# Optimization experiments

Hardware: AMD Instinct MI355X
Metric: run time of the kernel (lower is better)

The kernel has to match this reference:

```python
import jax, jax.numpy as jnp
import numpy as np

B, S, H, NH = 4, 2048, 512, 8
HD = H // NH  # head dim = 64


def setup_inputs() -> dict:
    key = jax.random.key(0)
    ks = jax.random.split(key, 12)
    f = lambda k, sh: jax.random.normal(k, sh, dtype=jnp.float32)
    w = lambda k: f(k, (H, H)) * 0.02  # Linear weight (out, in), torch-style
    return {
        "q": f(ks[0], (B, S, H)),
        "k": f(ks[1], (B, S, H)),
        "v": f(ks[2], (B, S, H)),
        "mask": jax.random.randint(ks[3], (B, S, S), 0, 2, dtype=jnp.int32),
        "Wq": w(ks[4]), "bq": jnp.zeros((H,), jnp.float32),
        "Wk": w(ks[5]), "bk": jnp.zeros((H,), jnp.float32),
        "Wv": w(ks[6]), "bv": jnp.zeros((H,), jnp.float32),
        "Wo": w(ks[7]), "bo": jnp.zeros((H,), jnp.float32),
    }


def reference(q, k, v, mask, Wq, bq, Wk, bk, Wv, bv, Wo, bo):
    b, s, h = q.shape
    scale = jnp.asarray(np.sqrt(HD), q.dtype)
    # QKV projections (torch Linear: x @ W.T + b), split into heads: b n s h
    def heads(x, W, bias):
        y = x @ W.T + bias
        return y.reshape(b, s, NH, HD).transpose(0, 2, 1, 3)
    Q = heads(q, Wq, bq)
    K = heads(k, Wk, bk)
    V = heads(v, Wv, bv)
    scores = jnp.einsum('bnsh,bnth->bnst', Q, K) / scale
    scores = jnp.where(mask[:, None, :, :] == 0, jnp.asarray(-1e9, scores.dtype), scores)
    attn = jax.nn.softmax(scores, axis=-1)
    # dropout is identity in eval mode
    out = jnp.einsum('bnst,bnth->bnsh', attn, V)
    out = out.transpose(0, 2, 1, 3).reshape(b, s, h)
    return out @ Wo.T + bo
```

## Files before the change

kernel.cpp:

```cpp
#include <hip/hip_runtime.h>
#include <cstdint>


typedef __bf16 bf16x8 __attribute__((ext_vector_type(8)));
typedef float  f32x4  __attribute__((ext_vector_type(4)));
typedef float  f32x16 __attribute__((ext_vector_type(16)));
typedef unsigned int uint32x2 __attribute__((ext_vector_type(2)));

#define MFMA16(a, b, c) __builtin_amdgcn_mfma_f32_16x16x32_bf16(a, b, c, 0, 0, 0)
#define MFMA32(a, b, c) __builtin_amdgcn_mfma_f32_32x32x16_bf16(a, b, c, 0, 0, 0)

__device__ __forceinline__ ushort f2bf(float f) {
  union { float f; uint32_t u; } v; v.f = f;
  return (ushort)((v.u + 0x8000u) >> 16);
}
__device__ __forceinline__ uint packbf(float a, float b) {
  union { float f; uint32_t u; } x, y; x.f = a; y.f = b;
#if __has_builtin(__builtin_amdgcn_perm)
  return __builtin_amdgcn_perm(y.u + 0x8000u, x.u + 0x8000u, 0x07060302u);
#else
  return ((x.u + 0x8000u) >> 16) | ((y.u + 0x8000u) & 0xffff0000u);
#endif
}
__device__ __forceinline__ uint cvtpk(float a, float b) {
  uint r;
  asm("v_cvt_pk_bf16_f32 %0, %1, %2" : "=v"(r) : "v"(a), "v"(b));
  return r;
}
__device__ __forceinline__ float exp2r(float x) {
#if __has_builtin(__builtin_amdgcn_exp2f)
  return __builtin_amdgcn_exp2f(x);
#else
  return exp2f(x);
#endif
}

typedef const __attribute__((address_space(1))) unsigned int* gas_u32;
typedef __attribute__((address_space(3))) unsigned int* las_u32;
__device__ __forceinline__ void gll16(const void* g, void* l) {
  __builtin_amdgcn_global_load_lds((gas_u32)g, (las_u32)l, 16, 0, 0);
}

__global__ __launch_bounds__(256) void cvt_w(
    const float* __restrict__ w0, const float* __restrict__ w1,
    const float* __restrict__ w2, const float* __restrict__ w3,
    ushort* __restrict__ dst) {
  const float* src = (blockIdx.y == 0) ? w0 : (blockIdx.y == 1) ? w1
                   : (blockIdx.y == 2) ? w2 : w3;
  ushort* d = dst + (size_t)blockIdx.y * 262144;
  int i = blockIdx.x * 256 + threadIdx.x;
  for (int j = i; j < 65536; j += 16384) {
    float4 v = ((const float4*)src)[j];
    uint2 o = { packbf(v.x, v.y), packbf(v.z, v.w) };
    ((uint2*)d)[j] = o;
  }
}

__global__ __launch_bounds__(256) void mask_bits_kernel(
    const int* __restrict__ mask, unsigned long long* __restrict__ MB) {
  const int lane = threadIdx.x & 63;
  const int wv = (int)((blockIdx.x * 256 + threadIdx.x) >> 6);
  const size_t base = (size_t)wv * 64;
  for (int j = 0; j < 64; j += 4) {
    int v0 = mask[(base + j + 0) * 64 + lane];
    int v1 = mask[(base + j + 1) * 64 + lane];
    int v2 = mask[(base + j + 2) * 64 + lane];
    int v3 = mask[(base + j + 3) * 64 + lane];
    unsigned long long b0 = __ballot(v0 != 0), b1 = __ballot(v1 != 0);
    unsigned long long b2 = __ballot(v2 != 0), b3 = __ballot(v3 != 0);
    if (lane == 0) {
      MB[base + j] = b0; MB[base + j + 1] = b1;
      MB[base + j + 2] = b2; MB[base + j + 3] = b3;
    }
  }
}

__global__ __launch_bounds__(256, 3) void qkv_gemm(
    const float* __restrict__ q, const float* __restrict__ k,
    const float* __restrict__ v, const ushort* __restrict__ Wb,
    const float* __restrict__ bq, const float* __restrict__ bk,
    const float* __restrict__ bv, ushort* __restrict__ Qh,
    ushort* __restrict__ Kh, ushort* __restrict__ Vt) {
  __shared__ ushort SH[128 * 136];
  __shared__ ushort Ws[128 * 64];
  float* Asf = (float*)SH;
  const int z = blockIdx.z;
  const float* X = (z == 0) ? q : (z == 1) ? k : v;
  const ushort* W = Wb + (size_t)z * 262144;
  const float* bias = (z == 0) ? bq : (z == 1) ? bk : bv;
  const float scale = (z == 0) ? 0.18033688011112042f : 1.0f;
  ushort* Y = (z == 0) ? Qh : (z == 1) ? Kh : Vt;

  const int tid = threadIdx.x, wv = tid >> 6, l = tid & 63;
  const int quad = l >> 4, ln = l & 15;
  const int m0 = blockIdx.x * 128, n0 = blockIdx.y * 128;
  const int wm = (wv & 1) * 64, wn = (wv >> 1) * 64;
  const int srA = l >> 4, sA = l & 15, cA = sA >> 1, hA = sA & 1;
  const int srW = l >> 3, scW = l & 7;
  f32x4 acc[4][4] = {};

  for (int kk = 0; kk < 512; kk += 64) {
#pragma unroll
    for (int i = 0; i < 8; ++i) {
      int rowa = wv * 32 + i * 4 + srA;
      gll16(X + (size_t)(m0 + rowa) * 512 + kk + ((cA ^ (rowa & 7)) * 8 + hA * 4),
            Asf + (wv * 32 + i * 4) * 64);
    }
#pragma unroll
    for (int i = 0; i < 4; ++i) {
      int roww = wv * 32 + i * 8 + srW;
      gll16(W + (size_t)(n0 + roww) * 512 + kk + ((scW ^ (roww & 7)) * 8),
            Ws + (wv * 32 + i * 8) * 64);
    }
    __syncthreads();
#pragma unroll
    for (int ks = 0; ks < 2; ++ks) {
      bf16x8 a[4], bw[4];
#pragma unroll
      for (int mt = 0; mt < 4; ++mt) {
        int row = wm + mt * 16 + ln;
        int p = (ks * 4 + quad) ^ (row & 7);
        const float* ap = &Asf[row * 64 + p * 8];
        f32x4 x0 = *(const f32x4*)ap;
        f32x4 x1 = *(const f32x4*)(ap + 4);
        union { uint u[4]; bf16x8 v; } t;
        t.u[0] = cvtpk(x0[0], x0[1]);
        t.u[1] = cvtpk(x0[2], x0[3]);
        t.u[2] = cvtpk(x1[0], x1[1]);
        t.u[3] = cvtpk(x1[2], x1[3]);
        a[mt] = t.v;
      }
#pragma unroll
      for (int nt = 0; nt < 4; ++nt) {
        int row = wn + nt * 16 + ln;
        bw[nt] = *(const bf16x8*)&Ws[row * 64 + (((ks * 4 + quad) ^ (row & 7)) * 8)];
      }
#pragma unroll
      for (int mt = 0; mt < 4; ++mt)
#pragma unroll
        for (int nt = 0; nt < 4; ++nt)
          acc[mt][nt] = MFMA16(a[mt], bw[nt], acc[mt][nt]);
    }
    __syncthreads();
  }
  float bval[4];
#pragma unroll
  for (int nt = 0; nt < 4; ++nt) bval[nt] = bias[n0 + wn + nt * 16 + ln];

  if (z == 2) {
    ushort* uT = SH;
#pragma unroll
    for (int nt = 0; nt < 4; ++nt) {
      int row = wn + nt * 16 + ln;
#pragma unroll
      for (int mt = 0; mt < 4; ++mt) {
        int mbase = wm + mt * 16 + quad * 4;
        uint2 pk = { cvtpk(acc[mt][nt][0] + bval[nt], acc[mt][nt][1] + bval[nt]),
                     cvtpk(acc[mt][nt][2] + bval[nt], acc[mt][nt][3] + bval[nt]) };
        int c = (mbase >> 3) ^ (row & 7);
        *(uint2*)&uT[row * 128 + c * 8 + (quad & 1) * 4] = pk;
      }
    }
    __syncthreads();
#pragma unroll
    for (int j = 0; j < 8; ++j) {
      int i = tid + j * 256;
      int row = i >> 4, cs = i & 15;
      int g = cs ^ (row & 7);
      uint4 d = *(const uint4*)&uT[row * 128 + cs * 8];
      int n = n0 + row, m = m0 + g * 8;
      int bb = m >> 11, s = m & 2047, h = n >> 6, hd = n & 63;
      *(uint4*)(Y + ((size_t)((bb * 8 + h) * 64 + hd)) * 2048 + s) = d;
    }
  } else {
    ushort* uM = SH;
#pragma unroll
    for (int mt = 0; mt < 4; ++mt)
#pragma unroll
      for (int nt = 0; nt < 4; ++nt) {
        int n = wn + nt * 16 + ln;
#pragma unroll
        for (int r = 0; r < 4; ++r) {
          int m = wm + mt * 16 + quad * 4 + r;
          uM[m * 136 + n] = f2bf((acc[mt][nt][r] + bval[nt]) * scale);
        }
      }
    __syncthreads();
#pragma unroll
    for (int j = 0; j < 8; ++j) {
      int i = tid + j * 256;
      int row = i >> 4, cs = i & 15;
      uint4 d = *(const uint4*)&uM[row * 136 + cs * 8];
      int m = m0 + row, n = n0 + cs * 8;
      int bb = m >> 11, s = m & 2047, h = n >> 6, hd = n & 63;
      *(uint4*)(Y + (((size_t)(bb * 8 + h) * 2048) + s) * 64 + hd) = d;
    }
  }
}

__global__ __launch_bounds__(256, 4) void attn(
    const ushort* __restrict__ Qh, const ushort* __restrict__ Kh,
    const ushort* __restrict__ Vt, const unsigned long long* __restrict__ MB,
    ushort* __restrict__ O) {
  __shared__ ushort SMEM[16384];
  ushort* Ks = SMEM;
  ushort* Vs = SMEM + 8192;
  const int tid = threadIdx.x, wv = tid >> 6, lane = tid & 63;
  const int hs = lane >> 5, lq = lane & 31;
  const int qh = wv >> 1, kvh = wv & 1;
  const int bh = blockIdx.x, qb = blockIdx.y;
  const size_t hoff = (size_t)bh * 2048 * 64;
  const int q0 = qb * 64;
  const int qg = q0 + qh * 32 + lq;
  const int srK = lane >> 3, scK = lane & 7;
  const int srV = lane >> 4, scV = lane & 15;

  bf16x8 qf[4];
#pragma unroll
  for (int ki = 0; ki < 4; ++ki)
    qf[ki] = *(const bf16x8*)(Qh + hoff + (size_t)qg * 64 + ki * 16 + hs * 8);

  bf16x8 ones;
#pragma unroll
  for (int j = 0; j < 8; ++j) ones[j] = (__bf16)1.0f;

  f32x16 po0 = {}, po1 = {};
  f32x16 lacc = {};
  const unsigned long long* mrow = MB + ((size_t)(bh >> 3) * 2048 + qg) * 32;

  for (int it = 0; it < 16; ++it) {
    const int kv0 = it * 128;
#pragma unroll
    for (int i = 0; i < 4; ++i) {
      int row = wv * 32 + i * 8 + srK;
      gll16(Kh + hoff + (size_t)(kv0 + row) * 64 + ((scK ^ (row & 7)) * 8),
            Ks + (wv * 32 + i * 8) * 64);
      int rv = wv * 16 + i * 4 + srV;
      gll16(Vt + hoff + (size_t)rv * 2048 + kv0 + ((scV ^ (rv & 7)) * 8),
            Vs + (wv * 16 + i * 4) * 128);
    }
    unsigned long long mbw = mrow[it * 2 + kvh];
    __syncthreads();

#pragma unroll
    for (int ch = 0; ch < 2; ++ch) {
      const int kvb = kvh * 64 + ch * 32;
      f32x16 sc_ = {};
#pragma unroll
      for (int ki = 0; ki < 4; ++ki) {
        int row = kvb + lq;
        bf16x8 ak = *(const bf16x8*)&Ks[row * 64 + (((2 * ki + hs) ^ (row & 7)) * 8)];
        sc_ = MFMA32(ak, qf[ki], sc_);
      }
      uint pk[8];
#pragma unroll
      for (int c = 0; c < 4; ++c) {
        unsigned nib = (unsigned)(mbw >> (ch * 32 + c * 8 + hs * 4)) & 0xFu;
        float p0 = (nib & 1u) ? exp2r(sc_[4 * c + 0]) : 0.f;
        float p1 = (nib & 2u) ? exp2r(sc_[4 * c + 1]) : 0.f;
        float p2 = (nib & 4u) ? exp2r(sc_[4 * c + 2]) : 0.f;
        float p3 = (nib & 8u) ? exp2r(sc_[4 * c + 3]) : 0.f;
        pk[2 * c + 0] = cvtpk(p0, p1);
        pk[2 * c + 1] = cvtpk(p2, p3);
      }
#pragma unroll
      for (int t2 = 0; t2 < 2; ++t2) {
        union { uint u[4]; bf16x8 v; } bp;
#if __has_builtin(__builtin_amdgcn_permlane32_swap)
        uint32x2 r02 = __builtin_amdgcn_permlane32_swap(pk[4 * t2 + 0], pk[4 * t2 + 2], false, false);
        uint32x2 r13 = __builtin_amdgcn_permlane32_swap(pk[4 * t2 + 1], pk[4 * t2 + 3], false, false);
        bp.u[0] = r02[0];
        bp.u[1] = r13[0];
        bp.u[2] = r02[1];
        bp.u[3] = r13[1];
#else
        uint bx0 = (uint)__shfl_xor((int)(hs ? pk[4 * t2 + 0] : pk[4 * t2 + 2]), 32);
        uint bx1 = (uint)__shfl_xor((int)(hs ? pk[4 * t2 + 1] : pk[4 * t2 + 3]), 32);
        bp.u[0] = hs ? bx0 : pk[4 * t2 + 0];
        bp.u[1] = hs ? bx1 : pk[4 * t2 + 1];
        bp.u[2] = hs ? pk[4 * t2 + 2] : bx0;
        bp.u[3] = hs ? pk[4 * t2 + 3] : bx1;
#endif
        lacc = MFMA32(ones, bp.v, lacc);
#pragma unroll
        for (int m2 = 0; m2 < 2; ++m2) {
          int hd = m2 * 32 + lq;
          int gch = (kvb >> 3) + 2 * t2 + hs;
          bf16x8 av = *(const bf16x8*)&Vs[hd * 128 + ((gch ^ (hd & 7)) * 8)];
          if (m2 == 0) po0 = MFMA32(av, bp.v, po0);
          else         po1 = MFMA32(av, bp.v, po1);
        }
      }
    }
    __syncthreads();
  }

  float l_own = lacc[0];
  float* psh = (float*)Ks;
  float* lsh = (float*)Vs;
  ushort* Osh = Vs + 256;
  if (kvh == 1) {
#pragma unroll
    for (int i = 0; i < 16; ++i) psh[(qh * 32 + i) * 64 + lane] = po0[i];
#pragma unroll
    for (int i = 0; i < 16; ++i) psh[(qh * 32 + 16 + i) * 64 + lane] = po1[i];
    lsh[qh * 64 + lane] = l_own;
  }
  __syncthreads();
  if (kvh == 0) {
    float linv = 1.0f / (l_own + lsh[qh * 64 + lane]);
    int row = qh * 32 + lq;
#pragma unroll
    for (int m2 = 0; m2 < 2; ++m2) {
#pragma unroll
      for (int c = 0; c < 4; ++c)
#pragma unroll
        for (int b2 = 0; b2 < 2; ++b2) {
          int r = 4 * c + 2 * b2;
          float v0, v1;
          if (m2 == 0) {
            v0 = (po0[r] + psh[(qh * 32 + r) * 64 + lane]) * linv;
            v1 = (po0[r + 1] + psh[(qh * 32 + r + 1) * 64 + lane]) * linv;
          } else {
            v0 = (po1[r] + psh[(qh * 32 + 16 + r) * 64 + lane]) * linv;
            v1 = (po1[r + 1] + psh[(qh * 32 + 16 + r + 1) * 64 + lane]) * linv;
          }
          int hd = m2 * 32 + 8 * c + 4 * hs + 2 * b2;
          *(uint*)&Osh[row * 72 + hd] = cvtpk(v0, v1);
        }
    }
  }
  __syncthreads();
  for (int i = tid; i < 512; i += 256) {
    int row = i >> 3, cc = i & 7;
    uint4 d = *(const uint4*)&Osh[row * 72 + cc * 8];
    *(uint4*)(O + ((size_t)((bh >> 3) * 2048 + q0 + row)) * 512 +
              (bh & 7) * 64 + cc * 8) = d;
  }
}

__global__ __launch_bounds__(256) void out_gemm(
    const ushort* __restrict__ X, const ushort* __restrict__ W,
    const float* __restrict__ bias, float* __restrict__ Y) {
  __shared__ ushort As[64 * 64];
  __shared__ ushort Ws[128 * 64];
  const int tid = threadIdx.x, wv = tid >> 6, l = tid & 63;
  const int quad = l >> 4, ln = l & 15;
  const int m0 = blockIdx.x * 64, n0 = blockIdx.y * 128;
  const int wm = (wv & 1) * 32, wn = (wv >> 1) * 64;
  const int sr = l >> 3, sc = l & 7;
  f32x4 acc[2][4] = {};
  for (int kk = 0; kk < 512; kk += 64) {
#pragma unroll
    for (int i = 0; i < 2; ++i) {
      int row = wv * 16 + i * 8 + sr;
      gll16(X + (size_t)(m0 + row) * 512 + kk + ((sc ^ (row & 7)) * 8),
            As + (wv * 16 + i * 8) * 64);
    }
#pragma unroll
    for (int i = 0; i < 4; ++i) {
      int row = wv * 32 + i * 8 + sr;
      gll16(W + (size_t)(n0 + row) * 512 + kk + ((sc ^ (row & 7)) * 8),
            Ws + (wv * 32 + i * 8) * 64);
    }
    __syncthreads();
#pragma unroll
    for (int ks = 0; ks < 2; ++ks) {
      bf16x8 a[2], bw[4];
#pragma unroll
      for (int mt = 0; mt < 2; ++mt) {
        int row = wm + mt * 16 + ln;
        a[mt] = *(const bf16x8*)&As[row * 64 + (((ks * 4 + quad) ^ (row & 7)) * 8)];
      }
#pragma unroll
      for (int nt = 0; nt < 4; ++nt) {
        int row = wn + nt * 16 + ln;
        bw[nt] = *(const bf16x8*)&Ws[row * 64 + (((ks * 4 + quad) ^ (row & 7)) * 8)];
      }
#pragma unroll
      for (int mt = 0; mt < 2; ++mt)
#pragma unroll
        for (int nt = 0; nt < 4; ++nt)
          acc[mt][nt] = MFMA16(a[mt], bw[nt], acc[mt][nt]);
    }
    __syncthreads();
  }
#pragma unroll
  for (int mt = 0; mt < 2; ++mt)
#pragma unroll
    for (int nt = 0; nt < 4; ++nt) {
      int n = n0 + wn + nt * 16 + ln;
      float bval = bias[n];
#pragma unroll
      for (int r = 0; r < 4; ++r) {
        int m = m0 + wm + mt * 16 + quad * 4 + r;
        Y[(size_t)m * 512 + n] = acc[mt][nt][r] + bval;
      }
    }
}

extern "C" void kernel_launch(void* const* d_in, const int* in_sizes, int n_in,
                              void* d_out, int out_size, void* d_ws, size_t ws_size,
                              hipStream_t stream) {
  const float* q    = (const float*)d_in[0];
  const float* k    = (const float*)d_in[1];
  const float* v    = (const float*)d_in[2];
  const int*   mask = (const int*)d_in[3];
  const float* Wq   = (const float*)d_in[4];
  const float* bq   = (const float*)d_in[5];
  const float* Wk   = (const float*)d_in[6];
  const float* bk   = (const float*)d_in[7];
  const float* Wv   = (const float*)d_in[8];
  const float* bv   = (const float*)d_in[9];
  const float* Wo   = (const float*)d_in[10];
  const float* bo   = (const float*)d_in[11];
  float* out = (float*)d_out;

  uint8_t* ws = (uint8_t*)d_ws;
  const size_t MiB = 1u << 20;
  ushort* Oh = (ushort*)(ws + 0 * MiB);
  ushort* Qh = (ushort*)(ws + 8 * MiB);
  ushort* Kh = (ushort*)(ws + 16 * MiB);
  ushort* Vt = (ushort*)(ws + 24 * MiB);
  unsigned long long* MB = (unsigned long long*)(ws + 32 * MiB);
  ushort* Wb = (ushort*)(ws + 34 * MiB);

  cvt_w<<<dim3(64, 4), 256, 0, stream>>>(Wq, Wk, Wv, Wo, Wb);
  mask_bits_kernel<<<1024, 256, 0, stream>>>(mask, MB);
  qkv_gemm<<<dim3(64, 4, 3), 256, 0, stream>>>(q, k, v, Wb, bq, bk, bv, Qh, Kh, Vt);
  attn<<<dim3(32, 32), 256, 0, stream>>>(Qh, Kh, Vt, MB, Oh);
  out_gemm<<<dim3(128, 4), 256, 0, stream>>>(Oh, Wb + 3 * 262144, bo, out);
}
```

Before: 251.3 us.

## Pre-convert q/k/v activations to bf16 before the QKV GEMM

Adds a separate pass that converts the fp32 q, k and v inputs to bf16 in workspace, so the QKV GEMM loads bf16 tiles straight into LDS instead of converting fp32 tiles per block. This halves the LDS footprint of the A tile. Launch bounds rise to 4 blocks per CU, and the Q/K epilogue is split into two 64-column halves that fit the smaller shared buffer. The cost is an extra kernel that reads 48 MB of fp32 and writes 24 MB of bf16, which removes the fp32 re-reads each GEMM block did across the four N tiles.

Result: slower. 261.5 us (+4.0%).

```diff
diff --git a/kernel.cpp b/kernel.cpp
--- a/kernel.cpp
+++ b/kernel.cpp
@@ -52,6 +52,19 @@
   for (int j = i; j < 65536; j += 16384) {
     float4 v = ((const float4*)src)[j];
     uint2 o = { packbf(v.x, v.y), packbf(v.z, v.w) };
+    ((uint2*)d)[j] = o;
+  }
+}
+
+__global__ __launch_bounds__(256) void cvt_x(
+    const float* __restrict__ q, const float* __restrict__ k,
+    const float* __restrict__ v, ushort* __restrict__ dst) {
+  const float* src = (blockIdx.y == 0) ? q : (blockIdx.y == 1) ? k : v;
+  ushort* d = dst + (size_t)blockIdx.y * 4194304;
+  int i = blockIdx.x * 256 + threadIdx.x;
+  for (int j = i; j < 1048576; j += 65536) {
+    float4 vv = ((const float4*)src)[j];
+    uint2 o = { cvtpk(vv.x, vv.y), cvtpk(vv.z, vv.w) };
     ((uint2*)d)[j] = o;
   }
 }
@@ -75,17 +88,16 @@
   }
 }
 
-__global__ __launch_bounds__(256, 3) void qkv_gemm(
-    const float* __restrict__ q, const float* __restrict__ k,
-    const float* __restrict__ v, const ushort* __restrict__ Wb,
+__global__ __launch_bounds__(256, 4) void qkv_gemm(
+    const ushort* __restrict__ Xb, const ushort* __restrict__ Wb,
     const float* __restrict__ bq, const float* __restrict__ bk,
     const float* __restrict__ bv, ushort* __restrict__ Qh,
     ushort* __restrict__ Kh, ushort* __restrict__ Vt) {
-  __shared__ ushort SH[128 * 136];
-  __shared__ ushort Ws[128 * 64];
-  float* Asf = (float*)SH;
+  __shared__ ushort SM[16384];
+  ushort* As = SM;
+  ushort* Wt = SM + 8192;
   const int z = blockIdx.z;
-  const float* X = (z == 0) ? q : (z == 1) ? k : v;
+  const ushort* X = Xb + (size_t)z * 4194304;
   const ushort* W = Wb + (size_t)z * 262144;
   const float* bias = (z == 0) ? bq : (z == 1) ? bk : bv;
   const float scale = (z == 0) ? 0.18033688011112042f : 1.0f;
@@ -95,22 +107,17 @@
   const int quad = l >> 4, ln = l & 15;
   const int m0 = blockIdx.x * 128, n0 = blockIdx.y * 128;
   const int wm = (wv & 1) * 64, wn = (wv >> 1) * 64;
-  const int srA = l >> 4, sA = l & 15, cA = sA >> 1, hA = sA & 1;
-  const int srW = l >> 3, scW = l & 7;
+  const int sr = l >> 3, sc = l & 7;
   f32x4 acc[4][4] = {};
 
   for (int kk = 0; kk < 512; kk += 64) {
 #pragma unroll
-    for (int i = 0; i < 8; ++i) {
-      int rowa = wv * 32 + i * 4 + srA;
-      gll16(X + (size_t)(m0 + rowa) * 512 + kk + ((cA ^ (rowa & 7)) * 8 + hA * 4),
-            Asf + (wv * 32 + i * 4) * 64);
-    }
-#pragma unroll
     for (int i = 0; i < 4; ++i) {
-      int roww = wv * 32 + i * 8 + srW;
-      gll16(W + (size_t)(n0 + roww) * 512 + kk + ((scW ^ (roww & 7)) * 8),
-            Ws + (wv * 32 + i * 8) * 64);
+      int row = wv * 32 + i * 8 + sr;
+      gll16(X + (size_t)(m0 + row) * 512 + kk + ((sc ^ (row & 7)) * 8),
+            As + (wv * 32 + i * 8) * 64);
+      gll16(W + (size_t)(n0 + row) * 512 + kk + ((sc ^ (row & 7)) * 8),
+            Wt + (wv * 32 + i * 8) * 64);
     }
     __syncthreads();
 #pragma unroll
@@ -119,21 +126,12 @@
 #pragma unroll
       for (int mt = 0; mt < 4; ++mt) {
         int row = wm + mt * 16 + ln;
-        int p = (ks * 4 + quad) ^ (row & 7);
-        const float* ap = &Asf[row * 64 + p * 8];
-        f32x4 x0 = *(const f32x4*)ap;
-        f32x4 x1 = *(const f32x4*)(ap + 4);
-        union { uint u[4]; bf16x8 v; } t;
-        t.u[0] = cvtpk(x0[0], x0[1]);
-        t.u[1] = cvtpk(x0[2], x0[3]);
-        t.u[2] = cvtpk(x1[0], x1[1]);
-        t.u[3] = cvtpk(x1[2], x1[3]);
-        a[mt] = t.v;
+        a[mt] = *(const bf16x8*)&As[row * 64 + (((ks * 4 + quad) ^ (row & 7)) * 8)];
       }
 #pragma unroll
       for (int nt = 0; nt < 4; ++nt) {
         int row = wn + nt * 16 + ln;
-        bw[nt] = *(const bf16x8*)&Ws[row * 64 + (((ks * 4 + quad) ^ (row & 7)) * 8)];
+        bw[nt] = *(const bf16x8*)&Wt[row * 64 + (((ks * 4 + quad) ^ (row & 7)) * 8)];
       }
 #pragma unroll
       for (int mt = 0; mt < 4; ++mt)
@@ -148,7 +146,7 @@
   for (int nt = 0; nt < 4; ++nt) bval[nt] = bias[n0 + wn + nt * 16 + ln];
 
   if (z == 2) {
-    ushort* uT = SH;
+    ushort* uT = SM;
 #pragma unroll
     for (int nt = 0; nt < 4; ++nt) {
       int row = wn + nt * 16 + ln;
@@ -173,27 +171,33 @@
       *(uint4*)(Y + ((size_t)((bb * 8 + h) * 64 + hd)) * 2048 + s) = d;
     }
   } else {
-    ushort* uM = SH;
-#pragma unroll
-    for (int mt = 0; mt < 4; ++mt)
-#pragma unroll
-      for (int nt = 0; nt < 4; ++nt) {
-        int n = wn + nt * 16 + ln;
-#pragma unroll
-        for (int r = 0; r < 4; ++r) {
-          int m = wm + mt * 16 + quad * 4 + r;
-          uM[m * 136 + n] = f2bf((acc[mt][nt][r] + bval[nt]) * scale);
-        }
-      }
-    __syncthreads();
-#pragma unroll
-    for (int j = 0; j < 8; ++j) {
-      int i = tid + j * 256;
-      int row = i >> 4, cs = i & 15;
-      uint4 d = *(const uint4*)&uM[row * 136 + cs * 8];
-      int m = m0 + row, n = n0 + cs * 8;
-      int bb = m >> 11, s = m & 2047, h = n >> 6, hd = n & 63;
-      *(uint4*)(Y + (((size_t)(bb * 8 + h) * 2048) + s) * 64 + hd) = d;
+    ushort* uM = SM;
+#pragma unroll
+    for (int half = 0; half < 2; ++half) {
+      __syncthreads();
+      if ((wv >> 1) == half) {
+#pragma unroll
+        for (int mt = 0; mt < 4; ++mt)
+#pragma unroll
+          for (int nt = 0; nt < 4; ++nt) {
+            int n = nt * 16 + ln;
+#pragma unroll
+            for (int r = 0; r < 4; ++r) {
+              int m = wm + mt * 16 + quad * 4 + r;
+              uM[m * 68 + n] = f2bf((acc[mt][nt][r] + bval[nt]) * scale);
+            }
+          }
+      }
+      __syncthreads();
+#pragma unroll
+      for (int j = 0; j < 4; ++j) {
+        int i = tid + j * 256;
+        int row = i >> 3, cs = i & 7;
+        uint4 d = *(const uint4*)&uM[row * 68 + cs * 8];
+        int m = m0 + row, n = n0 + half * 64 + cs * 8;
+        int bb = m >> 11, s = m & 2047, h = n >> 6, hd = n & 63;
+        *(uint4*)(Y + (((size_t)(bb * 8 + h) * 2048) + s) * 64 + hd) = d;
+      }
     }
   }
 }
@@ -424,10 +428,12 @@
   ushort* Vt = (ushort*)(ws + 24 * MiB);
   unsigned long long* MB = (unsigned long long*)(ws + 32 * MiB);
   ushort* Wb = (ushort*)(ws + 34 * MiB);
+  ushort* Xb = (ushort*)(ws + 36 * MiB);
 
   cvt_w<<<dim3(64, 4), 256, 0, stream>>>(Wq, Wk, Wv, Wo, Wb);
+  cvt_x<<<dim3(256, 3), 256, 0, stream>>>(q, k, v, Xb);
   mask_bits_kernel<<<1024, 256, 0, stream>>>(mask, MB);
-  qkv_gemm<<<dim3(64, 4, 3), 256, 0, stream>>>(q, k, v, Wb, bq, bk, bv, Qh, Kh, Vt);
+  qkv_gemm<<<dim3(64, 4, 3), 256, 0, stream>>>(Xb, Wb, bq, bk, bv, Qh, Kh, Vt);
   attn<<<dim3(32, 32), 256, 0, stream>>>(Qh, Kh, Vt, MB, Oh);
   out_gemm<<<dim3(128, 4), 256, 0, stream>>>(Oh, Wb + 3 * 262144, bo, out);
 }
```

## Double attention block to 128 query rows and fuse weight-convert with mask-pack

Applied to the files above, without the earlier changes.

The attention kernel now runs 512 threads (8 waves) per block covering 128 query rows, so each K/V tile staged in shared memory is reused by twice as many queries. The grid is halved and the cooperative load is split across more waves. The epilogue now does the split-KV reduction in two passes to fit the shared buffers. Separately, the weight bf16 conversion and the mask bit-packing are merged into one launch, which saves a kernel launch. The costs are more barriers, fewer blocks in flight, and register pressure from the launch_bounds(512,4) request.

After: 238.2 us. -5.2%, faster.

```diff
diff --git a/kernel.cpp b/kernel.cpp
--- a/kernel.cpp
+++ b/kernel.cpp
@@ -13,14 +13,6 @@
 __device__ __forceinline__ ushort f2bf(float f) {
   union { float f; uint32_t u; } v; v.f = f;
   return (ushort)((v.u + 0x8000u) >> 16);
-}
-__device__ __forceinline__ uint packbf(float a, float b) {
-  union { float f; uint32_t u; } x, y; x.f = a; y.f = b;
-#if __has_builtin(__builtin_amdgcn_perm)
-  return __builtin_amdgcn_perm(y.u + 0x8000u, x.u + 0x8000u, 0x07060302u);
-#else
-  return ((x.u + 0x8000u) >> 16) | ((y.u + 0x8000u) & 0xffff0000u);
-#endif
 }
 __device__ __forceinline__ uint cvtpk(float a, float b) {
   uint r;
@@ -41,26 +33,24 @@
   __builtin_amdgcn_global_load_lds((gas_u32)g, (las_u32)l, 16, 0, 0);
 }
 
-__global__ __launch_bounds__(256) void cvt_w(
+__global__ __launch_bounds__(256) void prep(
     const float* __restrict__ w0, const float* __restrict__ w1,
     const float* __restrict__ w2, const float* __restrict__ w3,
-    ushort* __restrict__ dst) {
-  const float* src = (blockIdx.y == 0) ? w0 : (blockIdx.y == 1) ? w1
-                   : (blockIdx.y == 2) ? w2 : w3;
-  ushort* d = dst + (size_t)blockIdx.y * 262144;
-  int i = blockIdx.x * 256 + threadIdx.x;
-  for (int j = i; j < 65536; j += 16384) {
-    float4 v = ((const float4*)src)[j];
-    uint2 o = { packbf(v.x, v.y), packbf(v.z, v.w) };
-    ((uint2*)d)[j] = o;
-  }
-}
-
-__global__ __launch_bounds__(256) void mask_bits_kernel(
+    ushort* __restrict__ Wb,
     const int* __restrict__ mask, unsigned long long* __restrict__ MB) {
-  const int lane = threadIdx.x & 63;
-  const int wv = (int)((blockIdx.x * 256 + threadIdx.x) >> 6);
-  const size_t base = (size_t)wv * 64;
+  const int tid = threadIdx.x, bid = blockIdx.x;
+  int i = bid * 256 + tid;
+  {
+    int wsel = i >> 16, j = i & 65535;
+    const float* src = (wsel == 0) ? w0 : (wsel == 1) ? w1
+                     : (wsel == 2) ? w2 : w3;
+    float4 vv = ((const float4*)src)[j];
+    uint2 o = { cvtpk(vv.x, vv.y), cvtpk(vv.z, vv.w) };
+    ((uint2*)(Wb + (size_t)wsel * 262144))[j] = o;
+  }
+  const int lane = tid & 63;
+  const int wvg = i >> 6;
+  const size_t base = (size_t)wvg * 64;
   for (int j = 0; j < 64; j += 4) {
     int v0 = mask[(base + j + 0) * 64 + lane];
     int v1 = mask[(base + j + 1) * 64 + lane];
@@ -198,7 +188,7 @@
   }
 }
 
-__global__ __launch_bounds__(256, 4) void attn(
+__global__ __launch_bounds__(512, 4) void attn(
     const ushort* __restrict__ Qh, const ushort* __restrict__ Kh,
     const ushort* __restrict__ Vt, const unsigned long long* __restrict__ MB,
     ushort* __restrict__ O) {
@@ -210,7 +200,7 @@
   const int qh = wv >> 1, kvh = wv & 1;
   const int bh = blockIdx.x, qb = blockIdx.y;
   const size_t hoff = (size_t)bh * 2048 * 64;
-  const int q0 = qb * 64;
+  const int q0 = qb * 128;
   const int qg = q0 + qh * 32 + lq;
   const int srK = lane >> 3, scK = lane & 7;
   const int srV = lane >> 4, scV = lane & 15;
@@ -231,13 +221,13 @@
   for (int it = 0; it < 16; ++it) {
     const int kv0 = it * 128;
 #pragma unroll
-    for (int i = 0; i < 4; ++i) {
-      int row = wv * 32 + i * 8 + srK;
+    for (int i = 0; i < 2; ++i) {
+      int row = wv * 16 + i * 8 + srK;
       gll16(Kh + hoff + (size_t)(kv0 + row) * 64 + ((scK ^ (row & 7)) * 8),
-            Ks + (wv * 32 + i * 8) * 64);
-      int rv = wv * 16 + i * 4 + srV;
+            Ks + (wv * 16 + i * 8) * 64);
+      int rv = wv * 8 + i * 4 + srV;
       gll16(Vt + hoff + (size_t)rv * 2048 + kv0 + ((scV ^ (rv & 7)) * 8),
-            Vs + (wv * 16 + i * 4) * 128);
+            Vs + (wv * 8 + i * 4) * 128);
     }
     unsigned long long mbw = mrow[it * 2 + kvh];
     __syncthreads();
@@ -299,43 +289,49 @@
   float* psh = (float*)Ks;
   float* lsh = (float*)Vs;
   ushort* Osh = Vs + 256;
-  if (kvh == 1) {
-#pragma unroll
-    for (int i = 0; i < 16; ++i) psh[(qh * 32 + i) * 64 + lane] = po0[i];
-#pragma unroll
-    for (int i = 0; i < 16; ++i) psh[(qh * 32 + 16 + i) * 64 + lane] = po1[i];
-    lsh[qh * 64 + lane] = l_own;
-  }
-  __syncthreads();
-  if (kvh == 0) {
-    float linv = 1.0f / (l_own + lsh[qh * 64 + lane]);
-    int row = qh * 32 + lq;
-#pragma unroll
-    for (int m2 = 0; m2 < 2; ++m2) {
-#pragma unroll
-      for (int c = 0; c < 4; ++c)
-#pragma unroll
-        for (int b2 = 0; b2 < 2; ++b2) {
-          int r = 4 * c + 2 * b2;
-          float v0, v1;
-          if (m2 == 0) {
-            v0 = (po0[r] + psh[(qh * 32 + r) * 64 + lane]) * linv;
-            v1 = (po0[r + 1] + psh[(qh * 32 + r + 1) * 64 + lane]) * linv;
-          } else {
-            v0 = (po1[r] + psh[(qh * 32 + 16 + r) * 64 + lane]) * linv;
-            v1 = (po1[r + 1] + psh[(qh * 32 + 16 + r + 1) * 64 + lane]) * linv;
+  const int qp = qh & 1;
+#pragma unroll
+  for (int p = 0; p < 2; ++p) {
+    if ((qh >> 1) == p && kvh == 1) {
+#pragma unroll
+      for (int i = 0; i < 16; ++i) psh[(qp * 32 + i) * 64 + lane] = po0[i];
+#pragma unroll
+      for (int i = 0; i < 16; ++i) psh[(qp * 32 + 16 + i) * 64 + lane] = po1[i];
+      lsh[qp * 64 + lane] = l_own;
+    }
+    __syncthreads();
+    if ((qh >> 1) == p && kvh == 0) {
+      float linv = 1.0f / (l_own + lsh[qp * 64 + lane]);
+      int row = qp * 32 + lq;
+#pragma unroll
+      for (int m2 = 0; m2 < 2; ++m2) {
+#pragma unroll
+        for (int c = 0; c < 4; ++c)
+#pragma unroll
+          for (int b2 = 0; b2 < 2; ++b2) {
+            int r = 4 * c + 2 * b2;
+            float v0, v1;
+            if (m2 == 0) {
+              v0 = (po0[r] + psh[(qp * 32 + r) * 64 + lane]) * linv;
+              v1 = (po0[r + 1] + psh[(qp * 32 + r + 1) * 64 + lane]) * linv;
+            } else {
+              v0 = (po1[r] + psh[(qp * 32 + 16 + r) * 64 + lane]) * linv;
+              v1 = (po1[r + 1] + psh[(qp * 32 + 16 + r + 1) * 64 + lane]) * linv;
+            }
+            int hd = m2 * 32 + 8 * c + 4 * hs + 2 * b2;
+            *(uint*)&Osh[row * 72 + hd] = cvtpk(v0, v1);
           }
-          int hd = m2 * 32 + 8 * c + 4 * hs + 2 * b2;
-          *(uint*)&Osh[row * 72 + hd] = cvtpk(v0, v1);
-        }
-    }
-  }
-  __syncthreads();
-  for (int i = tid; i < 512; i += 256) {
-    int row = i >> 3, cc = i & 7;
-    uint4 d = *(const uint4*)&Osh[row * 72 + cc * 8];
-    *(uint4*)(O + ((size_t)((bh >> 3) * 2048 + q0 + row)) * 512 +
-              (bh & 7) * 64 + cc * 8) = d;
+      }
+    }
+    __syncthreads();
+    {
+      int i = tid;
+      int row = i >> 3, cc = i & 7;
+      uint4 d = *(const uint4*)&Osh[row * 72 + cc * 8];
+      *(uint4*)(O + ((size_t)((bh >> 3) * 2048 + q0 + p * 64 + row)) * 512 +
+                (bh & 7) * 64 + cc * 8) = d;
+    }
+    __syncthreads();
   }
 }
 
@@ -425,9 +421,8 @@
   unsigned long long* MB = (unsigned long long*)(ws + 32 * MiB);
   ushort* Wb = (ushort*)(ws + 34 * MiB);
 
-  cvt_w<<<dim3(64, 4), 256, 0, stream>>>(Wq, Wk, Wv, Wo, Wb);
-  mask_bits_kernel<<<1024, 256, 0, stream>>>(mask, MB);
+  prep<<<1024, 256, 0, stream>>>(Wq, Wk, Wv, Wo, Wb, mask, MB);
   qkv_gemm<<<dim3(64, 4, 3), 256, 0, stream>>>(q, k, v, Wb, bq, bk, bv, Qh, Kh, Vt);
-  attn<<<dim3(32, 32), 256, 0, stream>>>(Qh, Kh, Vt, MB, Oh);
+  attn<<<dim3(32, 16), 512, 0, stream>>>(Qh, Kh, Vt, MB, Oh);
   out_gemm<<<dim3(128, 4), 256, 0, stream>>>(Oh, Wb + 3 * 262144, bo, out);
 }
```
